# Optimization experiments

Hardware: AMD Instinct MI355X
Metric: run time of the kernel (lower is better)

The kernel has to match this reference:

```python
import jax, jax.numpy as jnp
import numpy as np


def _gcn(h, W, b, src, dst):
    # PyG GCNConv: x @ W, then symmetric-normalized aggregation over edges
    # (edge list already includes self-loops), bias added after.
    n = h.shape[0]
    deg = jnp.zeros((n,), h.dtype).at[dst].add(jnp.ones((), h.dtype))
    dinv = jnp.where(deg > 0, jax.lax.rsqrt(deg), jnp.zeros((), h.dtype))
    norm = dinv[src] * dinv[dst]  # [E]
    m = h @ W                     # [N, d_h]
    out = jnp.zeros_like(m).at[dst].add(norm[:, None] * m[src])
    return out + b


def setup_inputs() -> dict:
    key = jax.random.key(0)
    F, K = 1000, 100              # files, blocks per file
    N = F * K                     # total blocks
    D_SEM, D_STR = 768, 256
    D_H, D_SH, D_PR, NPROJ = 512, 256, 256, 100

    # sliding-window (window=2) edges within each file, bidirectional, + self loops
    base = np.arange(N)
    pos = base % K
    s_l, d_l = [], []
    for d in (1, 2):
        i = base[pos < K - d]
        j = i + d
        s_l += [i, j]
        d_l += [j, i]
    s_l.append(base)  # self loops (GCNConv add_self_loops)
    d_l.append(base)
    src = jnp.asarray(np.concatenate(s_l), dtype=jnp.int32)
    dst = jnp.asarray(np.concatenate(d_l), dtype=jnp.int32)
    seg_ids = jnp.asarray(base // K, dtype=jnp.int32)  # file id per block (CSR blk_ptr equivalent)

    ks = jax.random.split(key, 16)
    def w(k, shape):
        return jax.random.normal(k, shape, jnp.float32) * 0.02
    z = lambda n: jnp.zeros((n,), jnp.float32)

    return dict(
        h_sem=jax.random.normal(ks[0], (N, D_SEM), jnp.float32),
        e_struct=jax.random.normal(ks[1], (N, D_STR), jnp.float32),
        W_fusion=w(ks[2], (D_SEM + D_STR, D_H)), b_fusion=z(D_H),
        W_g1=w(ks[3], (D_H, D_H)), b_g1=z(D_H),
        W_g2=w(ks[4], (D_H, D_H)), b_g2=z(D_H),
        W_att=w(ks[5], (D_H, D_H)), b_att=z(D_H),
        context=w(ks[6], (D_H,)),
        W_sh1=w(ks[7], (D_H, D_SH)), b_sh1=z(D_SH),
        W_sh2=w(ks[8], (D_SH, D_SH)), b_sh2=z(D_SH),
        W_pr1=w(ks[9], (D_H, D_PR)), b_pr1=z(D_PR),
        W_pr2=w(ks[10], (D_PR, D_PR)), b_pr2=z(D_PR),
        W_dpr=w(ks[11], (D_PR, NPROJ)), b_dpr=z(NPROJ),
        W_bug=w(ks[12], (D_H, 1)), b_bug=z(1),
        src=src, dst=dst, seg_ids=seg_ids, num_files=F,
    )


def reference(h_sem, e_struct, W_fusion, b_fusion, W_g1, b_g1, W_g2, b_g2,
              W_att, b_att, context, W_sh1, b_sh1, W_sh2, b_sh2,
              W_pr1, b_pr1, W_pr2, b_pr2, W_dpr, b_dpr, W_bug, b_bug,
              src, dst, seg_ids, num_files):
    # fusion of semantic + structural features
    h0 = jnp.concatenate([h_sem, e_struct], axis=1) @ W_fusion + b_fusion  # [N, d_h]
    h1 = jax.nn.relu(_gcn(h0, W_g1, b_g1, src, dst))
    h_blk = _gcn(h1, W_g2, b_g2, src, dst)                                # [N, d_h]

    # ragged attention pooling over per-file segments (vectorized segment softmax)
    scores = jnp.tanh(h_blk @ W_att + b_att) @ context                    # [N]
    seg_max = jax.ops.segment_max(scores, seg_ids, num_segments=num_files)
    ex = jnp.exp(scores - seg_max[seg_ids])
    seg_sum = jax.ops.segment_sum(ex, seg_ids, num_segments=num_files)
    alpha = ex / seg_sum[seg_ids]                                         # [N]
    h_file = jax.ops.segment_sum(alpha[:, None] * h_blk, seg_ids,
                                 num_segments=num_files)                  # [F, d_h]

    z_sh = jax.nn.relu(h_file @ W_sh1 + b_sh1) @ W_sh2 + b_sh2            # [F, d_sh]
    z_pr = jax.nn.relu(h_file @ W_pr1 + b_pr1) @ W_pr2 + b_pr2            # [F, d_pr]
    logits_pr_dom = z_pr @ W_dpr + b_dpr                                  # [F, num_projects]
    logit_bug = h_file @ W_bug + b_bug                                    # [F, 1]
    loss_ortho = jnp.mean((z_sh.T @ z_pr) ** 2)                           # disentanglement penalty
    return (h_blk, alpha, h_file, z_sh, z_pr, logits_pr_dom, logit_bug, loss_ortho)
```

## Files before the change

### kernel.cpp

```cpp
#include <hip/hip_runtime.h>

typedef unsigned short u16;
typedef unsigned int   u32;
typedef __attribute__((ext_vector_type(8))) short  short8;
typedef __attribute__((ext_vector_type(4))) float  floatx4;

#define DEV __device__ __forceinline__

DEV float bf2f(u16 u){ return __uint_as_float(((u32)u) << 16); }
DEV u16 f2bf(float x){
  u32 u = __float_as_uint(x);
  u += 0x7FFFu + ((u >> 16) & 1u);
  return (u16)(u >> 16);
}
DEV float blo(u32 u){ return __uint_as_float(u << 16); }
DEV float bhi(u32 u){ return __uint_as_float(u & 0xffff0000u); }

DEV void async16(const void* g, void* l){
  __builtin_amdgcn_global_load_lds((__attribute__((address_space(1))) void*)g,
                                   (__attribute__((address_space(3))) void*)l,
                                   16, 0, 0);
}

constexpr int NN   = 100000;
constexpr int FF   = 1000;
constexpr int KPF  = 100;
constexpr int DH   = 512;

constexpr size_t OUT_HBLK  = 0;
constexpr size_t OUT_ALPHA = 51200000;
constexpr size_t OUT_HFILE = 51300000;
constexpr size_t OUT_ZSH   = 51812000;
constexpr size_t OUT_ZPR   = 52068000;
constexpr size_t OUT_LOG   = 52324000;
constexpr size_t OUT_BUG   = 52424000;
constexpr size_t OUT_LOSS  = 52425000;

constexpr size_t WS_A      = 0;
constexpr size_t WS_M1     = 0;
constexpr size_t WS_H1     = 102400000;
constexpr size_t WS_HBLK   = 0;
constexpr size_t WS_H0     = 204800000;
constexpr size_t WS_M2     = 204800000;
constexpr size_t WS_SCOREP = 307200000;
constexpr size_t WS_WT     = 308800000;
constexpr size_t WS_HFILEB = 312300000;
constexpr size_t WS_TSH    = 313400000;
constexpr size_t WS_TPR    = 314000000;
constexpr size_t WS_ZPRB   = 314600000;
constexpr size_t WS_ORTHOP = 315200000;

constexpr int WT_FUS = 0;
constexpr int WT_G1  = 524288;
constexpr int WT_G2  = 786432;
constexpr int WT_ATT = 1048576;
constexpr int WT_SH1 = 1310720;
constexpr int WT_SH2 = 1441792;
constexpr int WT_PR1 = 1507328;
constexpr int WT_PR2 = 1638400;
constexpr int WT_DPR = 1703936;
constexpr int WT_TOT = 1729536;

struct PrepTab {
  const float* src[9];
  int K[9];
  int N[9];
  int prefix[10];
};

__global__ __launch_bounds__(256) void prep_w(PrepTab t, u16* __restrict__ dst){
  int gid = blockIdx.x * 256 + threadIdx.x;
  if (gid >= t.prefix[9]) return;
  int i = 0;
  while (gid >= t.prefix[i+1]) ++i;
  int e  = gid - t.prefix[i];
  int Ni = t.N[i];
  int k  = e / Ni;
  int n  = e - k * Ni;
  dst[t.prefix[i] + (size_t)n * t.K[i] + k] = f2bf(t.src[i][(size_t)k * Ni + n]);
}

__global__ __launch_bounds__(256) void build_A(const float* __restrict__ hsem,
                                               const float* __restrict__ est,
                                               u16* __restrict__ out){
  int gid = blockIdx.x * 256 + threadIdx.x;
  int row = gid >> 7;
  int c   = (gid & 127) << 3;
  const float* src = (c < 768) ? (hsem + (size_t)row * 768 + c)
                               : (est  + (size_t)row * 256 + (c - 768));
  float4 v0 = *(const float4*)src;
  float4 v1 = *(const float4*)(src + 4);
  uint4 o;
  o.x = (u32)f2bf(v0.x) | ((u32)f2bf(v0.y) << 16);
  o.y = (u32)f2bf(v0.z) | ((u32)f2bf(v0.w) << 16);
  o.z = (u32)f2bf(v1.x) | ((u32)f2bf(v1.y) << 16);
  o.w = (u32)f2bf(v1.z) | ((u32)f2bf(v1.w) << 16);
  *(uint4*)(out + (size_t)row * 1024 + c) = o;
}

template<int MODE, bool BIAS, bool RELU>
__global__ __launch_bounds__(256) void gemm_bt(
    const u16* __restrict__ A, const u16* __restrict__ B,
    int M, int N, int K,
    const float* __restrict__ bias,
    u16* __restrict__ outb, float* __restrict__ outf,
    int ldc, int nvalid,
    const float* __restrict__ ctx, float* __restrict__ scorep)
{
  __shared__ u16 As[128 * 32];
  __shared__ u16 Bs[128 * 32];
  const int tid  = threadIdx.x;
  const int wave = tid >> 6, lane = tid & 63;
  const int m0 = blockIdx.x * 128, n0 = blockIdx.y * 128;
  const int wm = (wave & 1) << 6, wn = (wave >> 1) << 6;
  const int lq = lane >> 4, lr = lane & 15;

  floatx4 acc[4][4];
  #pragma unroll
  for (int i = 0; i < 4; ++i)
    #pragma unroll
    for (int j = 0; j < 4; ++j)
      acc[i][j] = floatx4{0.f, 0.f, 0.f, 0.f};

  int arow = m0 + (wave << 4) + (lane >> 2);
  int ar0 = min(arow, M - 1);
  int ar1 = min(arow + 64, M - 1);
  int brow = n0 + (wave << 4) + (lane >> 2);
  int br0 = min(brow, N - 1);
  int br1 = min(brow + 64, N - 1);
  const int kc = (lane & 3) << 3;
  const u16* ga0 = A + (size_t)ar0 * K + kc;
  const u16* ga1 = A + (size_t)ar1 * K + kc;
  const u16* gb0 = B + (size_t)br0 * K + kc;
  const u16* gb1 = B + (size_t)br1 * K + kc;
  u16* la0 = As + (wave << 9);
  u16* la1 = As + 2048 + (wave << 9);
  u16* lb0 = Bs + (wave << 9);
  u16* lb1 = Bs + 2048 + (wave << 9);

  for (int it = 0, nIt = K >> 5; it < nIt; ++it) {
    async16(ga0, la0); async16(ga1, la1);
    async16(gb0, lb0); async16(gb1, lb1);
    ga0 += 32; ga1 += 32; gb0 += 32; gb1 += 32;
    __syncthreads();
    short8 af[4], bfr[4];
    #pragma unroll
    for (int mi = 0; mi < 4; ++mi)
      af[mi] = *(const short8*)(As + ((wm + mi * 16 + lr) << 5) + (lq << 3));
    #pragma unroll
    for (int ni = 0; ni < 4; ++ni)
      bfr[ni] = *(const short8*)(Bs + ((wn + ni * 16 + lr) << 5) + (lq << 3));
    #pragma unroll
    for (int mi = 0; mi < 4; ++mi)
      #pragma unroll
      for (int ni = 0; ni < 4; ++ni)
        acc[mi][ni] = __builtin_amdgcn_mfma_f32_16x16x32_bf16(af[mi], bfr[ni], acc[mi][ni], 0, 0, 0);
    __syncthreads();
  }

  if constexpr (MODE == 3) {
    #pragma unroll
    for (int mi = 0; mi < 4; ++mi) {
      #pragma unroll
      for (int r = 0; r < 4; ++r) {
        float p = 0.f;
        #pragma unroll
        for (int ni = 0; ni < 4; ++ni) {
          int gc = n0 + wn + ni * 16 + lr;
          p += tanhf(acc[mi][ni][r] + bias[gc]) * ctx[gc];
        }
        p += __shfl_xor(p, 1); p += __shfl_xor(p, 2);
        p += __shfl_xor(p, 4); p += __shfl_xor(p, 8);
        int gr = m0 + wm + mi * 16 + lq * 4 + r;
        if (lr == 0 && gr < M) scorep[(size_t)blockIdx.y * M + gr] = p;
      }
    }
  } else {
    #pragma unroll
    for (int mi = 0; mi < 4; ++mi) {
      int grb = m0 + wm + mi * 16 + lq * 4;
      #pragma unroll
      for (int ni = 0; ni < 4; ++ni) {
        int gc = n0 + wn + ni * 16 + lr;
        if (gc >= nvalid) continue;
        float bv = BIAS ? bias[gc] : 0.f;
        #pragma unroll
        for (int r = 0; r < 4; ++r) {
          int gr = grb + r;
          if (gr >= M) continue;
          float v = acc[mi][ni][r] + bv;
          if (RELU) v = fmaxf(v, 0.f);
          if (MODE == 0 || MODE == 2) outb[(size_t)gr * ldc + gc] = f2bf(v);
          if (MODE == 1 || MODE == 2) outf[(size_t)gr * ldc + gc] = v;
        }
      }
    }
  }
}

DEV float dinv_of(int p){
  return rsqrtf((float)(1 + min(p, 2) + min(99 - p, 2)));
}

template<bool RELU, bool DUAL>
__global__ __launch_bounds__(256) void agg_k(const u16* __restrict__ m,
                                             const float* __restrict__ bias,
                                             u16* __restrict__ outb,
                                             float* __restrict__ outf){
  int gid = blockIdx.x * 256 + threadIdx.x;
  int row = gid >> 6;
  int c   = (gid & 63) << 3;
  int pos = row % KPF;
  float ds = dinv_of(pos);
  float a0=0,a1=0,a2=0,a3=0,a4=0,a5=0,a6=0,a7=0;
  #pragma unroll
  for (int d = -2; d <= 2; ++d) {
    int p2 = pos + d;
    if (p2 < 0 || p2 >= KPF) continue;
    float w = ds * dinv_of(p2);
    uint4 v = *(const uint4*)(m + (size_t)(row + d) * DH + c);
    a0 += w * blo(v.x); a1 += w * bhi(v.x);
    a2 += w * blo(v.y); a3 += w * bhi(v.y);
    a4 += w * blo(v.z); a5 += w * bhi(v.z);
    a6 += w * blo(v.w); a7 += w * bhi(v.w);
  }
  float o[8] = {a0,a1,a2,a3,a4,a5,a6,a7};
  #pragma unroll
  for (int j = 0; j < 8; ++j) {
    o[j] += bias[c + j];
    if (RELU) o[j] = fmaxf(o[j], 0.f);
  }
  uint4 st;
  st.x = (u32)f2bf(o[0]) | ((u32)f2bf(o[1]) << 16);
  st.y = (u32)f2bf(o[2]) | ((u32)f2bf(o[3]) << 16);
  st.z = (u32)f2bf(o[4]) | ((u32)f2bf(o[5]) << 16);
  st.w = (u32)f2bf(o[6]) | ((u32)f2bf(o[7]) << 16);
  *(uint4*)(outb + (size_t)row * DH + c) = st;
  if (DUAL) {
    float4 f0 = {o[0], o[1], o[2], o[3]};
    float4 f1 = {o[4], o[5], o[6], o[7]};
    *(float4*)(outf + (size_t)row * DH + c)     = f0;
    *(float4*)(outf + (size_t)row * DH + c + 4) = f1;
  }
}

__global__ __launch_bounds__(256) void pool_k(const float* __restrict__ sp,
                                              const u16* __restrict__ hblk,
                                              float* __restrict__ alpha_out,
                                              float* __restrict__ hfile_f,
                                              u16* __restrict__ hfile_b){
  int f = blockIdx.x, tid = threadIdx.x;
  __shared__ float sAl[KPF];
  __shared__ float red[8];
  float s = -INFINITY;
  if (tid < KPF) {
    int r = f * KPF + tid;
    s = sp[r] + sp[NN + r] + sp[2 * NN + r] + sp[3 * NN + r];
  }
  float mx = s;
  for (int off = 32; off >= 1; off >>= 1) mx = fmaxf(mx, __shfl_xor(mx, off));
  if ((tid & 63) == 0) red[tid >> 6] = mx;
  __syncthreads();
  mx = fmaxf(fmaxf(red[0], red[1]), fmaxf(red[2], red[3]));
  float ex = (tid < KPF) ? expf(s - mx) : 0.f;
  float sm = ex;
  for (int off = 32; off >= 1; off >>= 1) sm += __shfl_xor(sm, off);
  if ((tid & 63) == 0) red[4 + (tid >> 6)] = sm;
  __syncthreads();
  sm = red[4] + red[5] + red[6] + red[7];
  float al = ex / sm;
  if (tid < KPF) { alpha_out[(size_t)f * KPF + tid] = al; sAl[tid] = al; }
  __syncthreads();
  const u16* base = hblk + (size_t)f * KPF * DH;
  float acc0 = 0.f, acc1 = 0.f;
  for (int i = 0; i < KPF; ++i) {
    float w = sAl[i];
    acc0 += w * bf2f(base[i * DH + tid]);
    acc1 += w * bf2f(base[i * DH + 256 + tid]);
  }
  hfile_f[(size_t)f * DH + tid]       = acc0;
  hfile_f[(size_t)f * DH + 256 + tid] = acc1;
  hfile_b[(size_t)f * DH + tid]       = f2bf(acc0);
  hfile_b[(size_t)f * DH + 256 + tid] = f2bf(acc1);
}

__global__ __launch_bounds__(256) void bug_k(const float* __restrict__ hfile,
                                             const float* __restrict__ w,
                                             const float* __restrict__ b,
                                             float* __restrict__ out){
  int row  = blockIdx.x * 4 + (threadIdx.x >> 6);
  int lane = threadIdx.x & 63;
  const float* h = hfile + (size_t)row * DH;
  float s = 0.f;
  #pragma unroll
  for (int j = 0; j < 8; ++j) s += h[lane + j * 64] * w[lane + j * 64];
  for (int off = 32; off >= 1; off >>= 1) s += __shfl_xor(s, off);
  if (lane == 0) out[row] = s + b[0];
}

__global__ __launch_bounds__(256) void ortho_k(const float* __restrict__ zsh,
                                               const float* __restrict__ zpr,
                                               float* __restrict__ part){
  int bi = blockIdx.x >> 4, bj = blockIdx.x & 15;
  int ty = threadIdx.x >> 4, tx = threadIdx.x & 15;
  __shared__ float sa[64 * 16], sb[64 * 16];
  float acc = 0.f;
  for (int k0 = 0; k0 < FF; k0 += 64) {
    #pragma unroll
    for (int q = 0; q < 4; ++q) {
      int kk = ty + q * 16;
      int k  = k0 + kk;
      float va = 0.f, vb = 0.f;
      if (k < FF) {
        va = zsh[(size_t)k * 256 + bi * 16 + tx];
        vb = zpr[(size_t)k * 256 + bj * 16 + tx];
      }
      sa[kk * 16 + tx] = va;
      sb[kk * 16 + tx] = vb;
    }
    __syncthreads();
    #pragma unroll 8
    for (int kk = 0; kk < 64; ++kk) acc += sa[kk * 16 + ty] * sb[kk * 16 + tx];
    __syncthreads();
  }
  float ssq = acc * acc;
  for (int off = 32; off >= 1; off >>= 1) ssq += __shfl_xor(ssq, off);
  __shared__ float r[4];
  if ((threadIdx.x & 63) == 0) r[threadIdx.x >> 6] = ssq;
  __syncthreads();
  if (threadIdx.x == 0) part[blockIdx.x] = r[0] + r[1] + r[2] + r[3];
}

__global__ __launch_bounds__(256) void ortho_fin(const float* __restrict__ part,
                                                 float* __restrict__ out){
  int tid = threadIdx.x;
  float s = part[tid];
  for (int off = 32; off >= 1; off >>= 1) s += __shfl_xor(s, off);
  __shared__ float r[4];
  if ((tid & 63) == 0) r[tid >> 6] = s;
  __syncthreads();
  if (tid == 0) out[0] = (r[0] + r[1] + r[2] + r[3]) * (1.0f / 65536.0f);
}

extern "C" void kernel_launch(void* const* d_in, const int* in_sizes, int n_in,
                              void* d_out, int out_size, void* d_ws, size_t ws_size,
                              hipStream_t stream) {
  const float* h_sem    = (const float*)d_in[0];
  const float* e_struct = (const float*)d_in[1];
  const float* W_fusion = (const float*)d_in[2];
  const float* b_fusion = (const float*)d_in[3];
  const float* W_g1     = (const float*)d_in[4];
  const float* b_g1     = (const float*)d_in[5];
  const float* W_g2     = (const float*)d_in[6];
  const float* b_g2     = (const float*)d_in[7];
  const float* W_att    = (const float*)d_in[8];
  const float* b_att    = (const float*)d_in[9];
  const float* context  = (const float*)d_in[10];
  const float* W_sh1    = (const float*)d_in[11];
  const float* b_sh1    = (const float*)d_in[12];
  const float* W_sh2    = (const float*)d_in[13];
  const float* b_sh2    = (const float*)d_in[14];
  const float* W_pr1    = (const float*)d_in[15];
  const float* b_pr1    = (const float*)d_in[16];
  const float* W_pr2    = (const float*)d_in[17];
  const float* b_pr2    = (const float*)d_in[18];
  const float* W_dpr    = (const float*)d_in[19];
  const float* b_dpr    = (const float*)d_in[20];
  const float* W_bug    = (const float*)d_in[21];
  const float* b_bug    = (const float*)d_in[22];

  char*  ws  = (char*)d_ws;
  float* out = (float*)d_out;

  u16*   Abf    = (u16*)(ws + WS_A);
  u16*   h0b    = (u16*)(ws + WS_H0);
  u16*   m1b    = (u16*)(ws + WS_M1);
  u16*   h1b    = (u16*)(ws + WS_H1);
  u16*   m2b    = (u16*)(ws + WS_M2);
  u16*   hblkb  = (u16*)(ws + WS_HBLK);
  float* scorep = (float*)(ws + WS_SCOREP);
  u16*   WT     = (u16*)(ws + WS_WT);
  u16*   hfileb = (u16*)(ws + WS_HFILEB);
  u16*   tshb   = (u16*)(ws + WS_TSH);
  u16*   tprb   = (u16*)(ws + WS_TPR);
  u16*   zprb   = (u16*)(ws + WS_ZPRB);
  float* opart  = (float*)(ws + WS_ORTHOP);

  PrepTab t;
  const float* srcs[9] = {W_fusion, W_g1, W_g2, W_att, W_sh1, W_sh2, W_pr1, W_pr2, W_dpr};
  int Ks[9] = {1024, 512, 512, 512, 512, 256, 512, 256, 256};
  int Ns[9] = {512, 512, 512, 512, 256, 256, 256, 256, 100};
  int pre[10] = {WT_FUS, WT_G1, WT_G2, WT_ATT, WT_SH1, WT_SH2, WT_PR1, WT_PR2, WT_DPR, WT_TOT};
  for (int i = 0; i < 9; ++i) { t.src[i] = srcs[i]; t.K[i] = Ks[i]; t.N[i] = Ns[i]; }
  for (int i = 0; i < 10; ++i) t.prefix[i] = pre[i];
  prep_w<<<(WT_TOT + 255) / 256, 256, 0, stream>>>(t, WT);

  build_A<<<NN * 128 / 256, 256, 0, stream>>>(h_sem, e_struct, Abf);

  gemm_bt<0, true, false><<<dim3(782, 4), 256, 0, stream>>>(
      Abf, WT + WT_FUS, NN, 512, 1024, b_fusion, h0b, nullptr, 512, 512, nullptr, nullptr);

  gemm_bt<0, false, false><<<dim3(782, 4), 256, 0, stream>>>(
      h0b, WT + WT_G1, NN, 512, 512, nullptr, m1b, nullptr, 512, 512, nullptr, nullptr);

  agg_k<true, false><<<NN * 64 / 256, 256, 0, stream>>>(m1b, b_g1, h1b, nullptr);

  gemm_bt<0, false, false><<<dim3(782, 4), 256, 0, stream>>>(
      h1b, WT + WT_G2, NN, 512, 512, nullptr, m2b, nullptr, 512, 512, nullptr, nullptr);

  agg_k<false, true><<<NN * 64 / 256, 256, 0, stream>>>(m2b, b_g2, hblkb, out + OUT_HBLK);

  gemm_bt<3, true, false><<<dim3(782, 4), 256, 0, stream>>>(
      hblkb, WT + WT_ATT, NN, 512, 512, b_att, nullptr, nullptr, 512, 512, context, scorep);

  pool_k<<<FF, 256, 0, stream>>>(scorep, hblkb, out + OUT_ALPHA, out + OUT_HFILE, hfileb);

  gemm_bt<0, true, true><<<dim3(8, 2), 256, 0, stream>>>(
      hfileb, WT + WT_SH1, FF, 256, 512, b_sh1, tshb, nullptr, 256, 256, nullptr, nullptr);
  gemm_bt<1, true, false><<<dim3(8, 2), 256, 0, stream>>>(
      tshb, WT + WT_SH2, FF, 256, 256, b_sh2, nullptr, out + OUT_ZSH, 256, 256, nullptr, nullptr);
  gemm_bt<0, true, true><<<dim3(8, 2), 256, 0, stream>>>(
      hfileb, WT + WT_PR1, FF, 256, 512, b_pr1, tprb, nullptr, 256, 256, nullptr, nullptr);
  gemm_bt<2, true, false><<<dim3(8, 2), 256, 0, stream>>>(
      tprb, WT + WT_PR2, FF, 256, 256, b_pr2, zprb, out + OUT_ZPR, 256, 256, nullptr, nullptr);
  gemm_bt<1, true, false><<<dim3(8, 1), 256, 0, stream>>>(
      zprb, WT + WT_DPR, FF, 100, 256, b_dpr, nullptr, out + OUT_LOG, 100, 100, nullptr, nullptr);

  bug_k<<<FF / 4, 256, 0, stream>>>(out + OUT_HFILE, W_bug, b_bug, out + OUT_BUG);

  ortho_k<<<256, 256, 0, stream>>>(out + OUT_ZSH, out + OUT_ZPR, opart);
  ortho_fin<<<1, 256, 0, stream>>>(opart, out + OUT_LOSS);
}
```

Baseline: 1.421 ms.

## Triple-buffer GEMM LDS loads, swizzle LDS layout, remap blocks across XCDs

The GEMM kernel now keeps three LDS stages and prefetches two K-tiles ahead. It uses explicit vmcnt waits and a single barrier per iteration in place of two __syncthreads, so global loads overlap with the MFMA work. The K-chunk offsets in LDS are XOR-swizzled to reduce bank conflicts on fragment reads. A 1D grid is remapped so that consecutive tiles (sharing A rows) land on the same XCD, which should improve L2 reuse. The cost is triple the LDS per block, which may lower occupancy, plus more delicate synchronisation.

```diff
diff --git a/kernel.cpp b/kernel.cpp
--- a/kernel.cpp
+++ b/kernel.cpp
@@ -101,17 +101,24 @@
 template<int MODE, bool BIAS, bool RELU>
 __global__ __launch_bounds__(256) void gemm_bt(
     const u16* __restrict__ A, const u16* __restrict__ B,
-    int M, int N, int K,
+    int M, int N, int K, int ny,
     const float* __restrict__ bias,
     u16* __restrict__ outb, float* __restrict__ outf,
     int ldc, int nvalid,
     const float* __restrict__ ctx, float* __restrict__ scorep)
 {
-  __shared__ u16 As[128 * 32];
-  __shared__ u16 Bs[128 * 32];
+  __shared__ u16 As[3 * 4096];
+  __shared__ u16 Bs[3 * 4096];
   const int tid  = threadIdx.x;
   const int wave = tid >> 6, lane = tid & 63;
-  const int m0 = blockIdx.x * 128, n0 = blockIdx.y * 128;
+
+  const int nwg = (int)gridDim.x;
+  const int q   = nwg >> 3, r = nwg & 7;
+  const int xcd = (int)blockIdx.x & 7, pos = (int)blockIdx.x >> 3;
+  const int lid = (xcd < r ? xcd * (q + 1) : r * (q + 1) + (xcd - r) * q) + pos;
+  const int ty  = lid % ny, tx = lid / ny;
+  const int m0  = tx << 7, n0 = ty << 7;
+
   const int wm = (wave & 1) << 6, wn = (wave >> 1) << 6;
   const int lq = lane >> 4, lr = lane & 15;
 
@@ -128,51 +135,65 @@
   int brow = n0 + (wave << 4) + (lane >> 2);
   int br0 = min(brow, N - 1);
   int br1 = min(brow + 64, N - 1);
-  const int kc = (lane & 3) << 3;
+  const int kc = (((lane & 3) ^ ((lane >> 3) & 3)) << 3);
   const u16* ga0 = A + (size_t)ar0 * K + kc;
   const u16* ga1 = A + (size_t)ar1 * K + kc;
   const u16* gb0 = B + (size_t)br0 * K + kc;
   const u16* gb1 = B + (size_t)br1 * K + kc;
-  u16* la0 = As + (wave << 9);
-  u16* la1 = As + 2048 + (wave << 9);
-  u16* lb0 = Bs + (wave << 9);
-  u16* lb1 = Bs + 2048 + (wave << 9);
-
-  for (int it = 0, nIt = K >> 5; it < nIt; ++it) {
-    async16(ga0, la0); async16(ga1, la1);
-    async16(gb0, lb0); async16(gb1, lb1);
+
+  auto STAGE = [&](int buf){
+    u16* as = As + (buf << 12);
+    u16* bs = Bs + (buf << 12);
+    async16(ga0, as + (wave << 9));
+    async16(ga1, as + 2048 + (wave << 9));
+    async16(gb0, bs + (wave << 9));
+    async16(gb1, bs + 2048 + (wave << 9));
     ga0 += 32; ga1 += 32; gb0 += 32; gb1 += 32;
-    __syncthreads();
+  };
+
+  const int nIt = K >> 5;
+  STAGE(0);
+  if (nIt > 1) STAGE(1);
+  const int rsw = (lr >> 1) & 3;
+  int bt = 0;
+  for (int it = 0; it < nIt; ++it) {
+    if (it + 1 < nIt) asm volatile("s_waitcnt vmcnt(4) lgkmcnt(0)" ::: "memory");
+    else              asm volatile("s_waitcnt vmcnt(0) lgkmcnt(0)" ::: "memory");
+    __builtin_amdgcn_s_barrier();
+    __builtin_amdgcn_sched_barrier(0);
+    if (it + 2 < nIt) { int b2 = bt + 2; if (b2 >= 3) b2 -= 3; STAGE(b2); }
+    const u16* as = As + (bt << 12);
+    const u16* bs = Bs + (bt << 12);
     short8 af[4], bfr[4];
     #pragma unroll
     for (int mi = 0; mi < 4; ++mi)
-      af[mi] = *(const short8*)(As + ((wm + mi * 16 + lr) << 5) + (lq << 3));
+      af[mi] = *(const short8*)(as + ((wm + mi * 16 + lr) << 5) + ((lq ^ rsw) << 3));
     #pragma unroll
     for (int ni = 0; ni < 4; ++ni)
-      bfr[ni] = *(const short8*)(Bs + ((wn + ni * 16 + lr) << 5) + (lq << 3));
+      bfr[ni] = *(const short8*)(bs + ((wn + ni * 16 + lr) << 5) + ((lq ^ rsw) << 3));
     #pragma unroll
     for (int mi = 0; mi < 4; ++mi)
       #pragma unroll
       for (int ni = 0; ni < 4; ++ni)
         acc[mi][ni] = __builtin_amdgcn_mfma_f32_16x16x32_bf16(af[mi], bfr[ni], acc[mi][ni], 0, 0, 0);
-    __syncthreads();
+    if (++bt == 3) bt = 0;
   }
 
   if constexpr (MODE == 3) {
     #pragma unroll
     for (int mi = 0; mi < 4; ++mi) {
       #pragma unroll
-      for (int r = 0; r < 4; ++r) {
+      for (int r2 = 0; r2 < 4; ++r2) {
         float p = 0.f;
         #pragma unroll
         for (int ni = 0; ni < 4; ++ni) {
           int gc = n0 + wn + ni * 16 + lr;
-          p += tanhf(acc[mi][ni][r] + bias[gc]) * ctx[gc];
+          p += tanhf(acc[mi][ni][r2] + bias[gc]) * ctx[gc];
         }
         p += __shfl_xor(p, 1); p += __shfl_xor(p, 2);
         p += __shfl_xor(p, 4); p += __shfl_xor(p, 8);
-        int gr = m0 + wm + mi * 16 + lq * 4 + r;
-        if (lr == 0 && gr < M) scorep[(size_t)blockIdx.y * M + gr] = p;
+        int gr = m0 + wm + mi * 16 + lq * 4 + r2;
+        if (lr == 0 && gr < M) scorep[(size_t)ty * M + gr] = p;
       }
     }
   } else {
@@ -185,10 +206,10 @@
         if (gc >= nvalid) continue;
         float bv = BIAS ? bias[gc] : 0.f;
         #pragma unroll
-        for (int r = 0; r < 4; ++r) {
-          int gr = grb + r;
+        for (int r2 = 0; r2 < 4; ++r2) {
+          int gr = grb + r2;
           if (gr >= M) continue;
-          float v = acc[mi][ni][r] + bv;
+          float v = acc[mi][ni][r2] + bv;
           if (RELU) v = fmaxf(v, 0.f);
           if (MODE == 0 || MODE == 2) outb[(size_t)gr * ldc + gc] = f2bf(v);
           if (MODE == 1 || MODE == 2) outf[(size_t)gr * ldc + gc] = v;
@@ -397,34 +418,34 @@
 
   build_A<<<NN * 128 / 256, 256, 0, stream>>>(h_sem, e_struct, Abf);
 
-  gemm_bt<0, true, false><<<dim3(782, 4), 256, 0, stream>>>(
-      Abf, WT + WT_FUS, NN, 512, 1024, b_fusion, h0b, nullptr, 512, 512, nullptr, nullptr);
-
-  gemm_bt<0, false, false><<<dim3(782, 4), 256, 0, stream>>>(
-      h0b, WT + WT_G1, NN, 512, 512, nullptr, m1b, nullptr, 512, 512, nullptr, nullptr);
+  gemm_bt<0, true, false><<<782 * 4, 256, 0, stream>>>(
+      Abf, WT + WT_FUS, NN, 512, 1024, 4, b_fusion, h0b, nullptr, 512, 512, nullptr, nullptr);
+
+  gemm_bt<0, false, false><<<782 * 4, 256, 0, stream>>>(
+      h0b, WT + WT_G1, NN, 512, 512, 4, nullptr, m1b, nullptr, 512, 512, nullptr, nullptr);
 
   agg_k<true, false><<<NN * 64 / 256, 256, 0, stream>>>(m1b, b_g1, h1b, nullptr);
 
-  gemm_bt<0, false, false><<<dim3(782, 4), 256, 0, stream>>>(
-      h1b, WT + WT_G2, NN, 512, 512, nullptr, m2b, nullptr, 512, 512, nullptr, nullptr);
+  gemm_bt<0, false, false><<<782 * 4, 256, 0, stream>>>(
+      h1b, WT + WT_G2, NN, 512, 512, 4, nullptr, m2b, nullptr, 512, 512, nullptr, nullptr);
 
   agg_k<false, true><<<NN * 64 / 256, 256, 0, stream>>>(m2b, b_g2, hblkb, out + OUT_HBLK);
 
-  gemm_bt<3, true, false><<<dim3(782, 4), 256, 0, stream>>>(
-      hblkb, WT + WT_ATT, NN, 512, 512, b_att, nullptr, nullptr, 512, 512, context, scorep);
+  gemm_bt<3, true, false><<<782 * 4, 256, 0, stream>>>(
+      hblkb, WT + WT_ATT, NN, 512, 512, 4, b_att, nullptr, nullptr, 512, 512, context, scorep);
 
   pool_k<<<FF, 256, 0, stream>>>(scorep, hblkb, out + OUT_ALPHA, out + OUT_HFILE, hfileb);
 
-  gemm_bt<0, true, true><<<dim3(8, 2), 256, 0, stream>>>(
-      hfileb, WT + WT_SH1, FF, 256, 512, b_sh1, tshb, nullptr, 256, 256, nullptr, nullptr);
-  gemm_bt<1, true, false><<<dim3(8, 2), 256, 0, stream>>>(
-      tshb, WT + WT_SH2, FF, 256, 256, b_sh2, nullptr, out + OUT_ZSH, 256, 256, nullptr, nullptr);
-  gemm_bt<0, true, true><<<dim3(8, 2), 256, 0, stream>>>(
-      hfileb, WT + WT_PR1, FF, 256, 512, b_pr1, tprb, nullptr, 256, 256, nullptr, nullptr);
-  gemm_bt<2, true, false><<<dim3(8, 2), 256, 0, stream>>>(
-      tprb, WT + WT_PR2, FF, 256, 256, b_pr2, zprb, out + OUT_ZPR, 256, 256, nullptr, nullptr);
-  gemm_bt<1, true, false><<<dim3(8, 1), 256, 0, stream>>>(
-      zprb, WT + WT_DPR, FF, 100, 256, b_dpr, nullptr, out + OUT_LOG, 100, 100, nullptr, nullptr);
+  gemm_bt<0, true, true><<<8 * 2, 256, 0, stream>>>(
+      hfileb, WT + WT_SH1, FF, 256, 512, 2, b_sh1, tshb, nullptr, 256, 256, nullptr, nullptr);
+  gemm_bt<1, true, false><<<8 * 2, 256, 0, stream>>>(
+      tshb, WT + WT_SH2, FF, 256, 256, 2, b_sh2, nullptr, out + OUT_ZSH, 256, 256, nullptr, nullptr);
+  gemm_bt<0, true, true><<<8 * 2, 256, 0, stream>>>(
+      hfileb, WT + WT_PR1, FF, 256, 512, 2, b_pr1, tprb, nullptr, 256, 256, nullptr, nullptr);
+  gemm_bt<2, true, false><<<8 * 2, 256, 0, stream>>>(
+      tprb, WT + WT_PR2, FF, 256, 256, 2, b_pr2, zprb, out + OUT_ZPR, 256, 256, nullptr, nullptr);
+  gemm_bt<1, true, false><<<8 * 1, 256, 0, stream>>>(
+      zprb, WT + WT_DPR, FF, 100, 256, 1, b_dpr, nullptr, out + OUT_LOG, 100, 100, nullptr, nullptr);
 
   bug_k<<<FF / 4, 256, 0, stream>>>(out + OUT_HFILE, W_bug, b_bug, out + OUT_BUG);
 
```

Result: faster. 1.377 ms (-3.1%).
